# Performance work log

Measured on AMD Instinct MI355X. Metric: run time of the kernel, lower is better.

Reference implementation:

```python
import jax, jax.numpy as jnp
import numpy as np
import math

B, S, D_MODEL, H, CLIP = 4, 1024, 1024, 16, 16
HEAD_DIM = D_MODEL // H
NEG = -1e6


def setup_inputs() -> dict:
    key = jax.random.key(0)
    ks = jax.random.split(key, 10)
    scale = 1.0 / math.sqrt(D_MODEL)
    return {
        "queries": jax.random.normal(ks[0], (B, S, D_MODEL), jnp.float32),
        "keys": jax.random.normal(ks[1], (B, S, D_MODEL), jnp.float32),
        "values": jax.random.normal(ks[2], (B, S, D_MODEL), jnp.float32),
        "valid_lens": jax.random.randint(ks[3], (B,), 1, S + 1),
        "Wq": jax.random.normal(ks[4], (D_MODEL, D_MODEL), jnp.float32) * scale,
        "Wk": jax.random.normal(ks[5], (D_MODEL, D_MODEL), jnp.float32) * scale,
        "Wv": jax.random.normal(ks[6], (D_MODEL, D_MODEL), jnp.float32) * scale,
        "Wo": jax.random.normal(ks[7], (D_MODEL, D_MODEL), jnp.float32) * scale,
        "Ek": jax.random.normal(ks[8], (2 * CLIP + 1, HEAD_DIM), jnp.float32),
        "Ev": jax.random.normal(ks[9], (2 * CLIP + 1, HEAD_DIM), jnp.float32),
    }


def _split_heads(x):
    # [B, S, D] -> [B*H, S, head_dim]
    b, s, _ = x.shape
    return x.reshape(b, s, H, HEAD_DIM).transpose(0, 2, 1, 3).reshape(b * H, s, HEAD_DIM)


def reference(queries, keys, values, valid_lens, Wq, Wk, Wv, Wo, Ek, Ev):
    q = _split_heads(queries @ Wq.T)  # [BH, S, d]
    k = _split_heads(keys @ Wk.T)
    v = _split_heads(values @ Wv.T)

    # relative-position tables, shared across batch and heads: [Sq, Sk, d]
    rng = jnp.arange(S)
    dist = jnp.clip(rng[None, :] - rng[:, None], -CLIP, CLIP) + CLIP
    pos_k = Ek[dist]
    pos_v = Ev[dist]

    scores = jnp.einsum('bqd,bkd->bqk', q, k) + jnp.einsum('bqd,qkd->bqk', q, pos_k)
    scores = scores / math.sqrt(HEAD_DIM)

    vl = jnp.repeat(valid_lens, H)  # [B*H]
    mask = jnp.arange(S)[None, None, :] < vl[:, None, None]
    attn = jax.nn.softmax(jnp.where(mask, scores, NEG), axis=-1)

    out = jnp.einsum('bqk,bkd->bqd', attn, v) + jnp.einsum('bqk,qkd->bqd', attn, pos_v)

    # merge heads: [B*H, S, d] -> [B, S, D]
    out = out.reshape(B, H, S, HEAD_DIM).transpose(0, 2, 1, 3).reshape(B, S, D_MODEL)
    return out @ Wo.T
```

## Files before the change

### kernel.cpp

```cpp
#include <hip/hip_runtime.h>


typedef __attribute__((ext_vector_type(8))) short short8;
typedef __attribute__((ext_vector_type(4))) float floatx4;

__device__ __forceinline__ unsigned short f2bf(float f) {
  union { float f; unsigned u; } v; v.f = f;
  return (unsigned short)((v.u + 0x7fffu + ((v.u >> 16) & 1u)) >> 16);
}
__device__ __forceinline__ unsigned packbf(float lo, float hi) {
  return ((unsigned)f2bf(hi) << 16) | (unsigned)f2bf(lo);
}

__device__ __forceinline__ void gld16(const void* g, void* l) {
  __builtin_amdgcn_global_load_lds(
      (const __attribute__((address_space(1))) unsigned*)g,
      (__attribute__((address_space(3))) unsigned*)l, 16, 0, 0);
}

#define WS_XQ  ((size_t)0)
#define WS_XK  ((size_t)4194304)
#define WS_XV  ((size_t)8388608)
#define WS_W   ((size_t)12582912)
#define WS_EKB ((size_t)16777216)
#define WS_EVT ((size_t)16781312)
#define WS_QB  ((size_t)16785408)
#define WS_KB  ((size_t)20979712)
#define WS_VT  ((size_t)25174016)
#define WS_OB  ((size_t)0)

__global__ __launch_bounds__(256) void convert_all_kernel(
    const float* __restrict__ q, const float* __restrict__ k,
    const float* __restrict__ v,
    const float* __restrict__ wq, const float* __restrict__ wk,
    const float* __restrict__ wv, const float* __restrict__ wo,
    const float* __restrict__ Ek, const float* __restrict__ Ev,
    const int* __restrict__ valid_lens, unsigned short* __restrict__ ws) {
  int z = blockIdx.z;
  if (z < 3) {
    const float* src = z == 0 ? q : (z == 1 ? k : v);
    unsigned short* dst = ws + (size_t)z * 4194304;
    size_t i = ((size_t)blockIdx.x * 256 + threadIdx.x) * 8;
    if (z > 0) {
      int b = (int)(i >> 20), s = (int)((i >> 10) & 1023);
      if (s >= valid_lens[b]) return;
    }
    float4 a = *(const float4*)(src + i);
    float4 bb = *(const float4*)(src + i + 4);
    uint4 o = { packbf(a.x, a.y), packbf(a.z, a.w), packbf(bb.x, bb.y), packbf(bb.z, bb.w) };
    *(uint4*)(dst + i) = o;
  } else if (z < 7) {
    if (blockIdx.x >= 512) return;
    const float* src = (z == 3) ? wq : (z == 4 ? wk : (z == 5 ? wv : wo));
    unsigned short* dst = ws + WS_W + (size_t)(z - 3) * 1048576;
    size_t i = ((size_t)blockIdx.x * 256 + threadIdx.x) * 8;
    float4 a = *(const float4*)(src + i);
    float4 bb = *(const float4*)(src + i + 4);
    uint4 o = { packbf(a.x, a.y), packbf(a.z, a.w), packbf(bb.x, bb.y), packbf(bb.z, bb.w) };
    *(uint4*)(dst + i) = o;
  } else {
    if (blockIdx.x >= 4) return;
    int gid = blockIdx.x * 256 + threadIdx.x;
    unsigned short* ekb = ws + WS_EKB;
    int i0 = gid * 8;
    unsigned short vals[8];
#pragma unroll
    for (int u = 0; u < 8; u++) {
      int i = i0 + u;
      if (i < 4096) {
        int t = i >> 6, d = i & 63;
        vals[u] = (t < 33) ? f2bf(Ek[t * 64 + d]) : (unsigned short)0;
      } else {
        int j = i - 4096;
        int d = j >> 6, t = j & 63;
        vals[u] = (t < 33) ? f2bf(Ev[t * 64 + d]) : (unsigned short)0;
      }
    }
    *(uint4*)(ekb + i0) = *(uint4*)vals;
  }
}

__device__ __forceinline__ void gemm128_body(
    const unsigned short* __restrict__ A, const unsigned short* __restrict__ W,
    unsigned short* __restrict__ Cb, float* __restrict__ Cf, int mode, float scale) {
  __shared__ unsigned short sA[128 * 32];
  __shared__ unsigned short sB[128 * 32];
  const int tid = threadIdx.x, wave = tid >> 6, lane = tid & 63;
  const int lr = lane & 15, lq = lane >> 4;
  const int wr = wave >> 1, wc = wave & 1;
  const int m0 = blockIdx.y * 128, n0 = blockIdx.x * 128;
  const int srow = lane >> 2, scol = (lane & 3) * 8;

  const unsigned short* gA0 = A + (size_t)(m0 + wave * 16 + srow) * 1024 + scol;
  const unsigned short* gA1 = gA0 + (size_t)64 * 1024;
  const unsigned short* gB0 = W + (size_t)(n0 + wave * 16 + srow) * 1024 + scol;
  const unsigned short* gB1 = gB0 + (size_t)64 * 1024;
  unsigned short* lA0 = sA + wave * 512;  unsigned short* lA1 = lA0 + 2048;
  unsigned short* lB0 = sB + wave * 512;  unsigned short* lB1 = lB0 + 2048;

  floatx4 acc[4][4];
#pragma unroll
  for (int mi = 0; mi < 4; mi++)
#pragma unroll
    for (int ni = 0; ni < 4; ni++) acc[mi][ni] = (floatx4){0.f, 0.f, 0.f, 0.f};

  for (int k0 = 0; k0 < 1024; k0 += 32) {
    gld16(gA0 + k0, lA0); gld16(gA1 + k0, lA1);
    gld16(gB0 + k0, lB0); gld16(gB1 + k0, lB1);
    __syncthreads();
    short8 af[4], bf[4];
#pragma unroll
    for (int mi = 0; mi < 4; mi++)
      af[mi] = *(const short8*)(sA + (wr * 64 + mi * 16 + lr) * 32 + lq * 8);
#pragma unroll
    for (int ni = 0; ni < 4; ni++)
      bf[ni] = *(const short8*)(sB + (wc * 64 + ni * 16 + lr) * 32 + lq * 8);
#pragma unroll
    for (int mi = 0; mi < 4; mi++)
#pragma unroll
      for (int ni = 0; ni < 4; ni++)
        acc[mi][ni] = __builtin_amdgcn_mfma_f32_16x16x32_bf16(af[mi], bf[ni], acc[mi][ni], 0, 0, 0);
    __syncthreads();
  }

  if (mode == 2) {
#pragma unroll
    for (int mi = 0; mi < 4; mi++)
#pragma unroll
      for (int ni = 0; ni < 4; ni++) {
        int col = n0 + wc * 64 + ni * 16 + lr;
        int h = col >> 6, d = col & 63;
        int rowg = m0 + wr * 64 + mi * 16 + lq * 4;
        int b = rowg >> 10, s = rowg & 1023;
        int bh = b * 16 + h;
        uint2 pk;
        pk.x = packbf(acc[mi][ni][0], acc[mi][ni][1]);
        pk.y = packbf(acc[mi][ni][2], acc[mi][ni][3]);
        size_t off = (size_t)bh * 65536
                   + (size_t)((s >> 6) * 8 + (d >> 4) * 2 + ((s >> 5) & 1)) * 512
                   + (size_t)((((s >> 3) & 3) * 16) + (d & 15)) * 8 + (s & 7);
        *(uint2*)(Cb + off) = pk;
      }
  } else if (mode == 1) {
#pragma unroll
    for (int mi = 0; mi < 4; mi++)
#pragma unroll
      for (int ni = 0; ni < 4; ni++)
#pragma unroll
        for (int r = 0; r < 4; r++) {
          int rowg = m0 + wr * 64 + mi * 16 + lq * 4 + r;
          int col = n0 + wc * 64 + ni * 16 + lr;
          int b = rowg >> 10, s = rowg & 1023;
          int h = col >> 6, d = col & 63;
          int bh = b * 16 + h;
          size_t off = (size_t)bh * 65536
                     + (size_t)((s >> 6) * 8 + ((s & 63) >> 4) * 2 + (d >> 5)) * 512
                     + (size_t)((((d & 31) >> 3) * 16) + (s & 15)) * 8 + (d & 7);
          Cb[off] = f2bf(acc[mi][ni][r]);
        }
  } else if (mode == 3) {
#pragma unroll
    for (int mi = 0; mi < 4; mi++)
#pragma unroll
      for (int ni = 0; ni < 4; ni++)
#pragma unroll
        for (int r = 0; r < 4; r++) {
          int row = m0 + wr * 64 + mi * 16 + lq * 4 + r;
          int col = n0 + wc * 64 + ni * 16 + lr;
          Cf[(size_t)row * 1024 + col] = acc[mi][ni][r];
        }
  } else {
#pragma unroll
    for (int mi = 0; mi < 4; mi++)
#pragma unroll
      for (int ni = 0; ni < 4; ni++)
#pragma unroll
        for (int r = 0; r < 4; r++) {
          int row = m0 + wr * 64 + mi * 16 + lq * 4 + r;
          int col = n0 + wc * 64 + ni * 16 + lr;
          Cb[(size_t)row * 1024 + col] = f2bf(acc[mi][ni][r] * scale);
        }
  }
}

__global__ __launch_bounds__(256, 3) void proj_qkv_kernel(
    unsigned short* __restrict__ ws, const int* __restrict__ valid_lens) {
  int z = blockIdx.z;
  if (z > 0) {
    int m0 = blockIdx.y * 128;
    if ((m0 & 1023) >= valid_lens[m0 >> 10]) return;
  }
  const unsigned short* A = ws + (size_t)z * 4194304;
  const unsigned short* W = ws + WS_W + (size_t)z * 1048576;
  unsigned short* Cb = (z == 0) ? ws + WS_QB : (z == 1 ? ws + WS_KB : ws + WS_VT);
  int mode = (z == 2) ? 2 : (z == 0 ? 0 : 1);
  float scale = (z == 0) ? (0.125f * 1.4426950408889634f) : 1.0f;
  gemm128_body(A, W, Cb, nullptr, mode, scale);
}

__global__ __launch_bounds__(256, 4) void out_proj_kernel(
    const unsigned short* __restrict__ Ob, const unsigned short* __restrict__ Wo,
    float* __restrict__ out) {
  __shared__ unsigned short sA[64 * 32];
  __shared__ unsigned short sB[128 * 32];
  const int tid = threadIdx.x, wave = tid >> 6, lane = tid & 63;
  const int lr = lane & 15, lq = lane >> 4;
  const int wr = wave >> 1, wc = wave & 1;
  const int m0 = blockIdx.y * 64, n0 = blockIdx.x * 128;
  const int srow = lane >> 2, scol = (lane & 3) * 8;

  const unsigned short* gA0 = Ob + (size_t)(m0 + wave * 16 + srow) * 1024 + scol;
  const unsigned short* gB0 = Wo + (size_t)(n0 + wave * 16 + srow) * 1024 + scol;
  const unsigned short* gB1 = gB0 + (size_t)64 * 1024;
  unsigned short* lA0 = sA + wave * 512;
  unsigned short* lB0 = sB + wave * 512;  unsigned short* lB1 = lB0 + 2048;

  floatx4 acc[2][4];
#pragma unroll
  for (int mi = 0; mi < 2; mi++)
#pragma unroll
    for (int ni = 0; ni < 4; ni++) acc[mi][ni] = (floatx4){0.f, 0.f, 0.f, 0.f};

  for (int k0 = 0; k0 < 1024; k0 += 32) {
    gld16(gA0 + k0, lA0);
    gld16(gB0 + k0, lB0); gld16(gB1 + k0, lB1);
    __syncthreads();
    short8 af[2], bf[4];
#pragma unroll
    for (int mi = 0; mi < 2; mi++)
      af[mi] = *(const short8*)(sA + (wr * 32 + mi * 16 + lr) * 32 + lq * 8);
#pragma unroll
    for (int ni = 0; ni < 4; ni++)
      bf[ni] = *(const short8*)(sB + (wc * 64 + ni * 16 + lr) * 32 + lq * 8);
#pragma unroll
    for (int mi = 0; mi < 2; mi++)
#pragma unroll
      for (int ni = 0; ni < 4; ni++)
        acc[mi][ni] = __builtin_amdgcn_mfma_f32_16x16x32_bf16(af[mi], bf[ni], acc[mi][ni], 0, 0, 0);
    __syncthreads();
  }

#pragma unroll
  for (int mi = 0; mi < 2; mi++)
#pragma unroll
    for (int ni = 0; ni < 4; ni++)
#pragma unroll
      for (int r = 0; r < 4; r++) {
        int row = m0 + wr * 32 + mi * 16 + lq * 4 + r;
        int col = n0 + wc * 64 + ni * 16 + lr;
        out[(size_t)row * 1024 + col] = acc[mi][ni][r];
      }
}

__global__ __launch_bounds__(64, 2) void attn_rpr_kernel(
    const unsigned short* __restrict__ Qb, const unsigned short* __restrict__ Kf,
    const unsigned short* __restrict__ Vf, const int* __restrict__ valid_lens,
    const unsigned short* __restrict__ Ekb, const unsigned short* __restrict__ Evtb,
    unsigned short* __restrict__ Ob) {
  __shared__ unsigned short sP[32 * 72];
  __shared__ float sQE[32 * 34];
  __shared__ float sW[32 * 34];

  const int lane = threadIdx.x;
  const int lr = lane & 15, lq = lane >> 4;
  const int x = blockIdx.x;
  const int rr = x >> 8, ss = x & 255;
  const int b = rr & 3;
  const int bh = b * 16 + (ss & 15);
  const int qx = ((rr >> 2) << 4) + (ss >> 4);
  const int vlen = valid_lens[b];
  const int i0 = qx * 32;
  const int colh = (bh & 15) * 64;
  const size_t bat = (size_t)b * 1024 * 1024;
  const int rbase = lq * 4;

  for (int i = lane; i < 32 * 34; i += 64) sW[i] = 0.f;

  const unsigned short* gQ = Qb + bat + (size_t)(i0 + lr) * 1024 + colh + lq * 8;
  short8 aq0[2], aq1[2];
#pragma unroll
  for (int g = 0; g < 2; g++) {
    aq0[g] = *(const short8*)(gQ + (size_t)g * 16 * 1024);
    aq1[g] = *(const short8*)(gQ + (size_t)g * 16 * 1024 + 32);
  }

#pragma unroll
  for (int ni = 0; ni < 3; ni++) {
    short8 be0 = *(const short8*)(Ekb + (ni * 16 + lr) * 64 + lq * 8);
    short8 be1 = *(const short8*)(Ekb + (ni * 16 + lr) * 64 + 32 + lq * 8);
    int t = ni * 16 + lr;
#pragma unroll
    for (int g = 0; g < 2; g++) {
      floatx4 aqe = (floatx4){0.f, 0.f, 0.f, 0.f};
      aqe = __builtin_amdgcn_mfma_f32_16x16x32_bf16(aq0[g], be0, aqe, 0, 0, 0);
      aqe = __builtin_amdgcn_mfma_f32_16x16x32_bf16(aq1[g], be1, aqe, 0, 0, 0);
      if (t < 33)
#pragma unroll
        for (int r = 0; r < 4; r++) sQE[(g * 16 + rbase + r) * 34 + t] = aqe[r];
    }
  }

  floatx4 acc_o[2][4];
#pragma unroll
  for (int g = 0; g < 2; g++)
#pragma unroll
    for (int nd = 0; nd < 4; nd++) acc_o[g][nd] = (floatx4){0.f, 0.f, 0.f, 0.f};
  float rs0[2][4] = {{0.f,0.f,0.f,0.f},{0.f,0.f,0.f,0.f}};
  float rs32[2][4] = {{0.f,0.f,0.f,0.f},{0.f,0.f,0.f,0.f}};

  const int vcl = vlen < 1024 ? vlen : 1024;
  const int kt_max = (vcl + 63) >> 6;

  const unsigned short* gKf = Kf + (size_t)bh * 65536 + lane * 8;
  const unsigned short* gVf = Vf + (size_t)bh * 65536 + lane * 8;

  for (int kt = 0; kt < kt_max; kt++) {
    const int j0 = kt * 64;

    short8 bk[4][2], bv[4][2];
#pragma unroll
    for (int ni = 0; ni < 4; ni++) {
      bk[ni][0] = *(const short8*)(gKf + (size_t)(kt * 8 + ni * 2 + 0) * 512);
      bk[ni][1] = *(const short8*)(gKf + (size_t)(kt * 8 + ni * 2 + 1) * 512);
    }
#pragma unroll
    for (int nd = 0; nd < 4; nd++) {
      bv[nd][0] = *(const short8*)(gVf + (size_t)(kt * 8 + nd * 2 + 0) * 512);
      bv[nd][1] = *(const short8*)(gVf + (size_t)(kt * 8 + nd * 2 + 1) * 512);
    }

    floatx4 accs[2][4];
    __builtin_amdgcn_s_setprio(1);
#pragma unroll
    for (int g = 0; g < 2; g++)
#pragma unroll
      for (int ni = 0; ni < 4; ni++) {
        accs[g][ni] = (floatx4){0.f, 0.f, 0.f, 0.f};
        accs[g][ni] = __builtin_amdgcn_mfma_f32_16x16x32_bf16(aq0[g], bk[ni][0], accs[g][ni], 0, 0, 0);
        accs[g][ni] = __builtin_amdgcn_mfma_f32_16x16x32_bf16(aq1[g], bk[ni][1], accs[g][ni], 0, 0, 0);
      }
    __builtin_amdgcn_s_setprio(0);

    const bool general = (j0 > i0 - 79) && (j0 < i0 + 47);
    if (!general) {
      const bool hi = (j0 >= i0 + 47);
      const int tconst = hi ? 32 : 0;
#pragma unroll
      for (int g = 0; g < 2; g++) {
        float qe[4];
#pragma unroll
        for (int r = 0; r < 4; r++) qe[r] = sQE[(g * 16 + rbase + r) * 34 + tconst];
#pragma unroll
        for (int ni = 0; ni < 4; ni++)
#pragma unroll
          for (int r = 0; r < 4; r++) {
            int j_g = j0 + ni * 16 + lr;
            float pv = (j_g < vlen) ? exp2f(accs[g][ni][r] + qe[r]) : 0.f;
            if (hi) rs32[g][r] += pv; else rs0[g][r] += pv;
            sP[(g * 16 + rbase + r) * 72 + ni * 16 + lr] = f2bf(pv);
          }
      }
    } else {
#pragma unroll
      for (int g = 0; g < 2; g++)
#pragma unroll
        for (int ni = 0; ni < 4; ni++)
#pragma unroll
          for (int r = 0; r < 4; r++) {
            int i_g = i0 + g * 16 + rbase + r;
            int j_g = j0 + ni * 16 + lr;
            int ddr = j_g - i_g;
            int t = ddr < -16 ? 0 : (ddr > 16 ? 32 : ddr + 16);
            float pv = (j_g < vlen) ? exp2f(accs[g][ni][r] + sQE[(g * 16 + rbase + r) * 34 + t]) : 0.f;
            if (ddr <= -16)      rs0[g][r]  += pv;
            else if (ddr >= 16)  rs32[g][r] += pv;
            else {
              int idx = (g * 16 + rbase + r) * 34 + t;
              sW[idx] += pv;
            }
            sP[(g * 16 + rbase + r) * 72 + ni * 16 + lr] = f2bf(pv);
          }
    }

    __builtin_amdgcn_s_setprio(1);
#pragma unroll
    for (int g = 0; g < 2; g++) {
      short8 ap0 = *(const short8*)(sP + (g * 16 + lr) * 72 + lq * 8);
      short8 ap1 = *(const short8*)(sP + (g * 16 + lr) * 72 + 32 + lq * 8);
#pragma unroll
      for (int nd = 0; nd < 4; nd++) {
        acc_o[g][nd] = __builtin_amdgcn_mfma_f32_16x16x32_bf16(ap0, bv[nd][0], acc_o[g][nd], 0, 0, 0);
        acc_o[g][nd] = __builtin_amdgcn_mfma_f32_16x16x32_bf16(ap1, bv[nd][1], acc_o[g][nd], 0, 0, 0);
      }
    }
    __builtin_amdgcn_s_setprio(0);
  }

#pragma unroll
  for (int x2 = 1; x2 < 16; x2 <<= 1)
#pragma unroll
    for (int g = 0; g < 2; g++)
#pragma unroll
      for (int r = 0; r < 4; r++) {
        rs0[g][r] += __shfl_xor(rs0[g][r], x2, 64);
        rs32[g][r] += __shfl_xor(rs32[g][r], x2, 64);
      }
  if (lr == 0)
#pragma unroll
    for (int g = 0; g < 2; g++)
#pragma unroll
      for (int r = 0; r < 4; r++) {
        sW[(g * 16 + rbase + r) * 34 + 0] += rs0[g][r];
        sW[(g * 16 + rbase + r) * 34 + 32] += rs32[g][r];
      }

  {
    int row = lane >> 2;
    int c0 = (lane & 3) * 16;
    unsigned* sP32 = (unsigned*)sP;
#pragma unroll
    for (int g = 0; g < 2; g++)
#pragma unroll
      for (int q = 0; q < 8; q++) {
        int t0 = c0 + 2 * q, t1 = t0 + 1;
        float w0 = (t0 < 33) ? sW[(g * 16 + row) * 34 + t0] : 0.f;
        float w1 = (t1 < 33) ? sW[(g * 16 + row) * 34 + t1] : 0.f;
        sP32[(g * 16 + row) * 36 + (c0 >> 1) + q] = packbf(w0, w1);
      }
  }
#pragma unroll
  for (int g = 0; g < 2; g++) {
    short8 aw0 = *(const short8*)(sP + (g * 16 + lr) * 72 + lq * 8);
    short8 aw1 = *(const short8*)(sP + (g * 16 + lr) * 72 + 32 + lq * 8);
#pragma unroll
    for (int nd = 0; nd < 4; nd++) {
      short8 be0 = *(const short8*)(Evtb + (nd * 16 + lr) * 64 + lq * 8);
      short8 be1 = *(const short8*)(Evtb + (nd * 16 + lr) * 64 + 32 + lq * 8);
      acc_o[g][nd] = __builtin_amdgcn_mfma_f32_16x16x32_bf16(aw0, be0, acc_o[g][nd], 0, 0, 0);
      acc_o[g][nd] = __builtin_amdgcn_mfma_f32_16x16x32_bf16(aw1, be1, acc_o[g][nd], 0, 0, 0);
    }
  }

#pragma unroll
  for (int g = 0; g < 2; g++) {
    float linv[4];
#pragma unroll
    for (int r = 0; r < 4; r++) {
      float l = 0.f;
#pragma unroll
      for (int t = 0; t < 33; t++) l += sW[(g * 16 + rbase + r) * 34 + t];
      linv[r] = 1.f / l;
    }
#pragma unroll
    for (int nd = 0; nd < 4; nd++)
#pragma unroll
      for (int r = 0; r < 4; r++) {
        int row = i0 + g * 16 + rbase + r;
        Ob[bat + (size_t)row * 1024 + colh + nd * 16 + lr] =
            f2bf(acc_o[g][nd][r] * linv[r]);
      }
  }
}

extern "C" void kernel_launch(void* const* d_in, const int* in_sizes, int n_in,
                              void* d_out, int out_size, void* d_ws, size_t ws_size,
                              hipStream_t stream) {
  const float* queries = (const float*)d_in[0];
  const float* keys    = (const float*)d_in[1];
  const float* values  = (const float*)d_in[2];
  const int* valid_lens = (const int*)d_in[3];
  const float* Wq = (const float*)d_in[4];
  const float* Wk = (const float*)d_in[5];
  const float* Wv = (const float*)d_in[6];
  const float* Wo = (const float*)d_in[7];
  const float* Ek = (const float*)d_in[8];
  const float* Ev = (const float*)d_in[9];
  float* out = (float*)d_out;
  unsigned short* ws = (unsigned short*)d_ws;

  convert_all_kernel<<<dim3(2048, 1, 8), 256, 0, stream>>>(
      queries, keys, values, Wq, Wk, Wv, Wo, Ek, Ev, valid_lens, ws);
  proj_qkv_kernel<<<dim3(8, 32, 3), 256, 0, stream>>>(ws, valid_lens);
  attn_rpr_kernel<<<dim3(2048), 64, 0, stream>>>(
      ws + WS_QB, ws + WS_KB, ws + WS_VT, valid_lens, ws + WS_EKB, ws + WS_EVT, ws + WS_OB);
  out_proj_kernel<<<dim3(8, 64), 256, 0, stream>>>(ws + WS_OB, ws + WS_W + 3145728, out);
}
```

Before: 196.2 us.

## Process 64 query rows per attention wave to reuse K/V loads

Each single-wave attention block now handles 64 query rows instead of 32, processed in two 32-row halves per key tile, so each K/V tile loaded from global memory feeds twice as many rows. The grid is halved to 1024 blocks, the shared buffers are doubled, and the general-band threshold is widened to match the taller tile. The goal is to cut redundant K/V global traffic. In exchange register pressure rises (launch bound min-blocks removed), there are fewer waves for latency hiding, and more tiles take the slower general relative-position path.

```diff
diff --git a/kernel.cpp b/kernel.cpp
--- a/kernel.cpp
+++ b/kernel.cpp
@@ -252,34 +252,34 @@
       }
 }
 
-__global__ __launch_bounds__(64, 2) void attn_rpr_kernel(
+__global__ __launch_bounds__(64) void attn_rpr_kernel(
     const unsigned short* __restrict__ Qb, const unsigned short* __restrict__ Kf,
     const unsigned short* __restrict__ Vf, const int* __restrict__ valid_lens,
     const unsigned short* __restrict__ Ekb, const unsigned short* __restrict__ Evtb,
     unsigned short* __restrict__ Ob) {
-  __shared__ unsigned short sP[32 * 72];
-  __shared__ float sQE[32 * 34];
-  __shared__ float sW[32 * 34];
+  __shared__ unsigned short sP[64 * 72];
+  __shared__ float sQE[64 * 34];
+  __shared__ float sW[64 * 34];
 
   const int lane = threadIdx.x;
   const int lr = lane & 15, lq = lane >> 4;
   const int x = blockIdx.x;
-  const int rr = x >> 8, ss = x & 255;
-  const int b = rr & 3;
+  const int b = x >> 8;
+  const int ss = x & 255;
   const int bh = b * 16 + (ss & 15);
-  const int qx = ((rr >> 2) << 4) + (ss >> 4);
+  const int qx = ss >> 4;
   const int vlen = valid_lens[b];
-  const int i0 = qx * 32;
+  const int i0 = qx * 64;
   const int colh = (bh & 15) * 64;
   const size_t bat = (size_t)b * 1024 * 1024;
   const int rbase = lq * 4;
 
-  for (int i = lane; i < 32 * 34; i += 64) sW[i] = 0.f;
+  for (int i = lane; i < 64 * 34; i += 64) sW[i] = 0.f;
 
   const unsigned short* gQ = Qb + bat + (size_t)(i0 + lr) * 1024 + colh + lq * 8;
-  short8 aq0[2], aq1[2];
-#pragma unroll
-  for (int g = 0; g < 2; g++) {
+  short8 aq0[4], aq1[4];
+#pragma unroll
+  for (int g = 0; g < 4; g++) {
     aq0[g] = *(const short8*)(gQ + (size_t)g * 16 * 1024);
     aq1[g] = *(const short8*)(gQ + (size_t)g * 16 * 1024 + 32);
   }
@@ -290,7 +290,7 @@
     short8 be1 = *(const short8*)(Ekb + (ni * 16 + lr) * 64 + 32 + lq * 8);
     int t = ni * 16 + lr;
 #pragma unroll
-    for (int g = 0; g < 2; g++) {
+    for (int g = 0; g < 4; g++) {
       floatx4 aqe = (floatx4){0.f, 0.f, 0.f, 0.f};
       aqe = __builtin_amdgcn_mfma_f32_16x16x32_bf16(aq0[g], be0, aqe, 0, 0, 0);
       aqe = __builtin_amdgcn_mfma_f32_16x16x32_bf16(aq1[g], be1, aqe, 0, 0, 0);
@@ -300,13 +300,16 @@
     }
   }
 
-  floatx4 acc_o[2][4];
-#pragma unroll
-  for (int g = 0; g < 2; g++)
+  floatx4 acc_o[4][4];
+#pragma unroll
+  for (int g = 0; g < 4; g++)
 #pragma unroll
     for (int nd = 0; nd < 4; nd++) acc_o[g][nd] = (floatx4){0.f, 0.f, 0.f, 0.f};
-  float rs0[2][4] = {{0.f,0.f,0.f,0.f},{0.f,0.f,0.f,0.f}};
-  float rs32[2][4] = {{0.f,0.f,0.f,0.f},{0.f,0.f,0.f,0.f}};
+  float rs0[4][4], rs32[4][4];
+#pragma unroll
+  for (int g = 0; g < 4; g++)
+#pragma unroll
+    for (int r = 0; r < 4; r++) { rs0[g][r] = 0.f; rs32[g][r] = 0.f; }
 
   const int vcl = vlen < 1024 ? vlen : 1024;
   const int kt_max = (vcl + 63) >> 6;
@@ -329,77 +332,87 @@
       bv[nd][1] = *(const short8*)(gVf + (size_t)(kt * 8 + nd * 2 + 1) * 512);
     }
 
-    floatx4 accs[2][4];
-    __builtin_amdgcn_s_setprio(1);
-#pragma unroll
-    for (int g = 0; g < 2; g++)
-#pragma unroll
-      for (int ni = 0; ni < 4; ni++) {
-        accs[g][ni] = (floatx4){0.f, 0.f, 0.f, 0.f};
-        accs[g][ni] = __builtin_amdgcn_mfma_f32_16x16x32_bf16(aq0[g], bk[ni][0], accs[g][ni], 0, 0, 0);
-        accs[g][ni] = __builtin_amdgcn_mfma_f32_16x16x32_bf16(aq1[g], bk[ni][1], accs[g][ni], 0, 0, 0);
-      }
-    __builtin_amdgcn_s_setprio(0);
-
-    const bool general = (j0 > i0 - 79) && (j0 < i0 + 47);
-    if (!general) {
-      const bool hi = (j0 >= i0 + 47);
-      const int tconst = hi ? 32 : 0;
-#pragma unroll
-      for (int g = 0; g < 2; g++) {
-        float qe[4];
-#pragma unroll
-        for (int r = 0; r < 4; r++) qe[r] = sQE[(g * 16 + rbase + r) * 34 + tconst];
-#pragma unroll
-        for (int ni = 0; ni < 4; ni++)
-#pragma unroll
-          for (int r = 0; r < 4; r++) {
-            int j_g = j0 + ni * 16 + lr;
-            float pv = (j_g < vlen) ? exp2f(accs[g][ni][r] + qe[r]) : 0.f;
-            if (hi) rs32[g][r] += pv; else rs0[g][r] += pv;
-            sP[(g * 16 + rbase + r) * 72 + ni * 16 + lr] = f2bf(pv);
-          }
-      }
-    } else {
-#pragma unroll
-      for (int g = 0; g < 2; g++)
-#pragma unroll
-        for (int ni = 0; ni < 4; ni++)
-#pragma unroll
-          for (int r = 0; r < 4; r++) {
-            int i_g = i0 + g * 16 + rbase + r;
-            int j_g = j0 + ni * 16 + lr;
-            int ddr = j_g - i_g;
-            int t = ddr < -16 ? 0 : (ddr > 16 ? 32 : ddr + 16);
-            float pv = (j_g < vlen) ? exp2f(accs[g][ni][r] + sQE[(g * 16 + rbase + r) * 34 + t]) : 0.f;
-            if (ddr <= -16)      rs0[g][r]  += pv;
-            else if (ddr >= 16)  rs32[g][r] += pv;
-            else {
-              int idx = (g * 16 + rbase + r) * 34 + t;
-              sW[idx] += pv;
+    const bool general = (j0 > i0 - 79) && (j0 < i0 + 79);
+    const bool hi = (j0 >= i0 + 79);
+
+#pragma unroll
+    for (int p = 0; p < 2; p++) {
+      const int g0 = 2 * p;
+
+      floatx4 accs[2][4];
+      __builtin_amdgcn_s_setprio(1);
+#pragma unroll
+      for (int gg = 0; gg < 2; gg++)
+#pragma unroll
+        for (int ni = 0; ni < 4; ni++) {
+          accs[gg][ni] = (floatx4){0.f, 0.f, 0.f, 0.f};
+          accs[gg][ni] = __builtin_amdgcn_mfma_f32_16x16x32_bf16(aq0[g0 + gg], bk[ni][0], accs[gg][ni], 0, 0, 0);
+          accs[gg][ni] = __builtin_amdgcn_mfma_f32_16x16x32_bf16(aq1[g0 + gg], bk[ni][1], accs[gg][ni], 0, 0, 0);
+        }
+      __builtin_amdgcn_s_setprio(0);
+
+      if (!general) {
+        const int tconst = hi ? 32 : 0;
+#pragma unroll
+        for (int gg = 0; gg < 2; gg++) {
+          const int g = g0 + gg;
+          float qe[4];
+#pragma unroll
+          for (int r = 0; r < 4; r++) qe[r] = sQE[(g * 16 + rbase + r) * 34 + tconst];
+#pragma unroll
+          for (int ni = 0; ni < 4; ni++)
+#pragma unroll
+            for (int r = 0; r < 4; r++) {
+              int j_g = j0 + ni * 16 + lr;
+              float pv = (j_g < vlen) ? exp2f(accs[gg][ni][r] + qe[r]) : 0.f;
+              if (hi) rs32[g][r] += pv; else rs0[g][r] += pv;
+              sP[(g * 16 + rbase + r) * 72 + ni * 16 + lr] = f2bf(pv);
             }
-            sP[(g * 16 + rbase + r) * 72 + ni * 16 + lr] = f2bf(pv);
-          }
-    }
-
-    __builtin_amdgcn_s_setprio(1);
-#pragma unroll
-    for (int g = 0; g < 2; g++) {
-      short8 ap0 = *(const short8*)(sP + (g * 16 + lr) * 72 + lq * 8);
-      short8 ap1 = *(const short8*)(sP + (g * 16 + lr) * 72 + 32 + lq * 8);
-#pragma unroll
-      for (int nd = 0; nd < 4; nd++) {
-        acc_o[g][nd] = __builtin_amdgcn_mfma_f32_16x16x32_bf16(ap0, bv[nd][0], acc_o[g][nd], 0, 0, 0);
-        acc_o[g][nd] = __builtin_amdgcn_mfma_f32_16x16x32_bf16(ap1, bv[nd][1], acc_o[g][nd], 0, 0, 0);
-      }
-    }
-    __builtin_amdgcn_s_setprio(0);
+        }
+      } else {
+#pragma unroll
+        for (int gg = 0; gg < 2; gg++) {
+          const int g = g0 + gg;
+#pragma unroll
+          for (int ni = 0; ni < 4; ni++)
+#pragma unroll
+            for (int r = 0; r < 4; r++) {
+              int i_g = i0 + g * 16 + rbase + r;
+              int j_g = j0 + ni * 16 + lr;
+              int ddr = j_g - i_g;
+              int t = ddr < -16 ? 0 : (ddr > 16 ? 32 : ddr + 16);
+              float pv = (j_g < vlen) ? exp2f(accs[gg][ni][r] + sQE[(g * 16 + rbase + r) * 34 + t]) : 0.f;
+              if (ddr <= -16)      rs0[g][r]  += pv;
+              else if (ddr >= 16)  rs32[g][r] += pv;
+              else {
+                int idx = (g * 16 + rbase + r) * 34 + t;
+                sW[idx] += pv;
+              }
+              sP[(g * 16 + rbase + r) * 72 + ni * 16 + lr] = f2bf(pv);
+            }
+        }
+      }
+
+      __builtin_amdgcn_s_setprio(1);
+#pragma unroll
+      for (int gg = 0; gg < 2; gg++) {
+        const int g = g0 + gg;
+        short8 ap0 = *(const short8*)(sP + (g * 16 + lr) * 72 + lq * 8);
+        short8 ap1 = *(const short8*)(sP + (g * 16 + lr) * 72 + 32 + lq * 8);
+#pragma unroll
+        for (int nd = 0; nd < 4; nd++) {
+          acc_o[g][nd] = __builtin_amdgcn_mfma_f32_16x16x32_bf16(ap0, bv[nd][0], acc_o[g][nd], 0, 0, 0);
+          acc_o[g][nd] = __builtin_amdgcn_mfma_f32_16x16x32_bf16(ap1, bv[nd][1], acc_o[g][nd], 0, 0, 0);
+        }
+      }
+      __builtin_amdgcn_s_setprio(0);
+    }
   }
 
 #pragma unroll
   for (int x2 = 1; x2 < 16; x2 <<= 1)
 #pragma unroll
-    for (int g = 0; g < 2; g++)
+    for (int g = 0; g < 4; g++)
 #pragma unroll
       for (int r = 0; r < 4; r++) {
         rs0[g][r] += __shfl_xor(rs0[g][r], x2, 64);
@@ -407,7 +420,7 @@
       }
   if (lr == 0)
 #pragma unroll
-    for (int g = 0; g < 2; g++)
+    for (int g = 0; g < 4; g++)
 #pragma unroll
       for (int r = 0; r < 4; r++) {
         sW[(g * 16 + rbase + r) * 34 + 0] += rs0[g][r];
@@ -419,7 +432,7 @@
     int c0 = (lane & 3) * 16;
     unsigned* sP32 = (unsigned*)sP;
 #pragma unroll
-    for (int g = 0; g < 2; g++)
+    for (int g = 0; g < 4; g++)
 #pragma unroll
       for (int q = 0; q < 8; q++) {
         int t0 = c0 + 2 * q, t1 = t0 + 1;
@@ -429,7 +442,7 @@
       }
   }
 #pragma unroll
-  for (int g = 0; g < 2; g++) {
+  for (int g = 0; g < 4; g++) {
     short8 aw0 = *(const short8*)(sP + (g * 16 + lr) * 72 + lq * 8);
     short8 aw1 = *(const short8*)(sP + (g * 16 + lr) * 72 + 32 + lq * 8);
 #pragma unroll
@@ -442,7 +455,7 @@
   }
 
 #pragma unroll
-  for (int g = 0; g < 2; g++) {
+  for (int g = 0; g < 4; g++) {
     float linv[4];
 #pragma unroll
     for (int r = 0; r < 4; r++) {
@@ -481,7 +494,7 @@
   convert_all_kernel<<<dim3(2048, 1, 8), 256, 0, stream>>>(
       queries, keys, values, Wq, Wk, Wv, Wo, Ek, Ev, valid_lens, ws);
   proj_qkv_kernel<<<dim3(8, 32, 3), 256, 0, stream>>>(ws, valid_lens);
-  attn_rpr_kernel<<<dim3(2048), 64, 0, stream>>>(
+  attn_rpr_kernel<<<dim3(1024), 64, 0, stream>>>(
       ws + WS_QB, ws + WS_KB, ws + WS_VT, valid_lens, ws + WS_EKB, ws + WS_EVT, ws + WS_OB);
   out_proj_kernel<<<dim3(8, 64), 256, 0, stream>>>(ws + WS_OB, ws + WS_W + 3145728, out);
 }
```

Result: slower. 226.1 us (+15.2%).
